# Performance work log

Hardware: AMD Instinct MI355X
Metric: run time of the kernel (lower is better)

## Reference

```python
import jax, jax.numpy as jnp
import numpy as np

NQ = 4            # num_qubits
DIM = 2 ** NQ     # 16-dim complex state

def _rx(theta):
    c = jnp.cos(theta / 2.0); s = jnp.sin(theta / 2.0)
    return jnp.array([[c, -1j * s], [-1j * s, c]], dtype=jnp.complex64)

def _ry(theta):
    c = jnp.cos(theta / 2.0); s = jnp.sin(theta / 2.0)
    return jnp.array([[c, -s], [s, c]], dtype=jnp.complex64)

def _apply_1q(state, q, U):
    # state: [B, 16] complex; apply 2x2 unitary U on qubit q (qubit 0 = MSB)
    B = state.shape[0]
    st = state.reshape((B,) + (2,) * NQ)
    st = jnp.moveaxis(st, 1 + q, -1)
    st = st @ U.T
    st = jnp.moveaxis(st, -1, 1 + q)
    return st.reshape(B, DIM)

def _apply_cnot(state, c, t):
    # flip target qubit t where control qubit c == 1
    B = state.shape[0]
    st = state.reshape((B,) + (2,) * NQ)
    st = jnp.moveaxis(st, (1 + c, 1 + t), (-2, -1))
    st = jnp.stack([st[..., 0, :], st[..., 1, ::-1]], axis=-2)
    st = jnp.moveaxis(st, (-2, -1), (1 + c, 1 + t))
    return st.reshape(B, DIM)

def _circuit(state):
    rx1, ry1 = _rx(0.1), _ry(0.2)
    rx2, ry2 = _rx(0.3), _ry(0.4)
    for q in range(NQ):
        state = _apply_1q(state, q, rx1)
        state = _apply_1q(state, q, ry1)
    for q in range(NQ - 1):
        state = _apply_cnot(state, q, q + 1)
    for q in range(NQ):
        state = _apply_1q(state, q, rx2)
        state = _apply_1q(state, q, ry2)
    return state

def setup_inputs() -> dict:
    key = jax.random.key(0)
    ks = jax.random.split(key, 9)
    B = 65536
    return {
        'x':   jax.random.normal(ks[0], (B, 784), dtype=jnp.float32),
        'We1': jax.random.normal(ks[1], (784, 256), dtype=jnp.float32) * 0.05,
        'be1': jnp.zeros((256,), dtype=jnp.float32),
        'We2': jax.random.normal(ks[2], (256, 32), dtype=jnp.float32) * 0.05,
        'be2': jnp.zeros((32,), dtype=jnp.float32),
        'W1':  jax.random.normal(ks[3], (32, 128), dtype=jnp.float32) * 0.05,
        'b1':  jnp.zeros((128,), dtype=jnp.float32),
        'W2':  jax.random.normal(ks[4], (128, 10), dtype=jnp.float32) * 0.05,
        'b2':  jnp.zeros((10,), dtype=jnp.float32),
    }

def reference(x, We1, be1, We2, be2, W1, b1, W2, b2):
    # encoder: Linear(784,256) -> ReLU -> Linear(256,32) -> Tanh
    h = jax.nn.relu(x @ We1 + be1)
    enc = jnp.tanh(h @ We2 + be2)               # [B, 32]
    psi = (enc[:, :DIM] + 1j * enc[:, DIM:]).astype(jnp.complex64)
    norm = jnp.sqrt(jnp.sum(jnp.abs(psi) ** 2, axis=1, keepdims=True))
    psi = psi / norm
    psi = _circuit(psi)                          # [B, 16] complex
    feat = jnp.concatenate([psi.real, psi.imag], axis=1)  # [B, 32]
    # classifier: Linear(32,128) -> ReLU -> (Dropout=identity in eval) -> Linear(128,10)
    out = jax.nn.relu(feat @ W1 + b1) @ W2 + b2
    return out
```

## Files before the change

kernel.cpp:

```cpp
#include <hip/hip_runtime.h>
#include <stdint.h>

#define DEVINL __device__ __forceinline__

typedef short bf16x8 __attribute__((ext_vector_type(8)));
typedef float f32x4  __attribute__((ext_vector_type(4)));

DEVINL uint16_t f2bf(float f) {
    uint32_t u = __builtin_bit_cast(uint32_t, f);
    uint32_t r = u + 0x7fffu + ((u >> 16) & 1u);
    return (uint16_t)(r >> 16);
}

DEVINL f32x4 mfma16x16x32(bf16x8 a, bf16x8 b, f32x4 c) {
    return __builtin_amdgcn_mfma_f32_16x16x32_bf16(a, b, c, 0, 0, 0);
}

#define WS_WE1T 0
#define WS_H    401408
#define WS_WE2T 33955840
#define WS_W1T  33972224
#define WS_W2T  33980416

__global__ __launch_bounds__(256) void prep_weights(
    const float* __restrict__ We1, const float* __restrict__ We2,
    const float* __restrict__ W1,  const float* __restrict__ W2,
    uint16_t* __restrict__ We1T, uint16_t* __restrict__ We2T,
    uint16_t* __restrict__ W1T,  uint16_t* __restrict__ W2T) {
    int tid = blockIdx.x * 256 + threadIdx.x;
    if (tid < 256 * 784) {
        int n = tid / 784, k = tid % 784;
        We1T[tid] = f2bf(We1[k * 256 + n]);
        return;
    }
    int t2 = tid - 256 * 784;
    if (t2 < 32 * 256) {
        int n = t2 / 256, k = t2 % 256;
        We2T[t2] = f2bf(We2[k * 32 + n]);
        return;
    }
    int t3 = t2 - 32 * 256;
    if (t3 < 128 * 32) {
        int n = t3 / 32, k = t3 % 32;
        W1T[t3] = f2bf(W1[k * 128 + n]);
        return;
    }
    int t4 = t3 - 128 * 32;
    if (t4 < 16 * 128) {
        int n = t4 / 128, k = t4 % 128;
        W2T[t4] = (n < 10) ? f2bf(W2[k * 10 + n]) : (uint16_t)0;
        return;
    }
}

__global__ __launch_bounds__(512) void gemm1_kernel(
    const float* __restrict__ x, const uint16_t* __restrict__ We1T,
    const float* __restrict__ be1, uint16_t* __restrict__ h) {
    __shared__ __align__(16) uint16_t Als[128 * 40];
    __shared__ __align__(16) uint16_t Bls[256 * 40];

    const int t = threadIdx.x;
    const int mbase = blockIdx.x * 128;
    const int w  = t >> 6;
    const int l  = t & 63;
    const int wm = w >> 2;
    const int wn = w & 3;
    const int lm = l & 15;
    const int lq = l >> 4;

    f32x4 acc[4][4] = {};

    const int ar = t >> 2;
    const int aq = t & 3;
    const int br = t >> 1;
    const int bh = t & 1;

    for (int k0 = 0; k0 < 784; k0 += 32) {
        {
            float4 v0 = {0.f,0.f,0.f,0.f}, v1 = {0.f,0.f,0.f,0.f};
            int c = k0 + aq * 8;
            if (c < 784) {
                const float* p = x + (size_t)(mbase + ar) * 784 + c;
                v0 = *(const float4*)p;
                v1 = *(const float4*)(p + 4);
            }
            union { uint4 u4; uint16_t us[8]; } pk;
            pk.us[0] = f2bf(v0.x); pk.us[1] = f2bf(v0.y);
            pk.us[2] = f2bf(v0.z); pk.us[3] = f2bf(v0.w);
            pk.us[4] = f2bf(v1.x); pk.us[5] = f2bf(v1.y);
            pk.us[6] = f2bf(v1.z); pk.us[7] = f2bf(v1.w);
            *(uint4*)&Als[ar * 40 + aq * 8] = pk.u4;
        }
        {
            int c = k0 + bh * 16;
            uint4 u0 = {0,0,0,0}, u1 = {0,0,0,0};
            if (c < 784) {
                const uint16_t* p = We1T + (size_t)br * 784 + c;
                u0 = *(const uint4*)p;
                u1 = *(const uint4*)(p + 8);
            }
            *(uint4*)&Bls[br * 40 + bh * 16]     = u0;
            *(uint4*)&Bls[br * 40 + bh * 16 + 8] = u1;
        }
        __syncthreads();

        bf16x8 afr[4], bfr[4];
        #pragma unroll
        for (int mi = 0; mi < 4; mi++)
            afr[mi] = *(const bf16x8*)&Als[(wm * 64 + mi * 16 + lm) * 40 + lq * 8];
        #pragma unroll
        for (int ni = 0; ni < 4; ni++)
            bfr[ni] = *(const bf16x8*)&Bls[(wn * 64 + ni * 16 + lm) * 40 + lq * 8];
        #pragma unroll
        for (int mi = 0; mi < 4; mi++)
            #pragma unroll
            for (int ni = 0; ni < 4; ni++)
                acc[mi][ni] = mfma16x16x32(afr[mi], bfr[ni], acc[mi][ni]);
        __syncthreads();
    }

    #pragma unroll
    for (int ni = 0; ni < 4; ni++) {
        int n = wn * 64 + ni * 16 + lm;
        float bias = be1[n];
        #pragma unroll
        for (int mi = 0; mi < 4; mi++) {
            #pragma unroll
            for (int i = 0; i < 4; i++) {
                int m = mbase + wm * 64 + mi * 16 + lq * 4 + i;
                float v = acc[mi][ni][i] + bias;
                v = v > 0.f ? v : 0.f;
                h[(size_t)m * 256 + n] = f2bf(v);
            }
        }
    }
}

DEVINL void apply_rx(float* sr, float* si, int bit, float c, float s) {
    #pragma unroll
    for (int i = 0; i < 16; i++) {
        if (!(i & bit)) {
            int j = i | bit;
            float r0 = sr[i], i0 = si[i], r1 = sr[j], i1 = si[j];
            sr[i] = c * r0 + s * i1;  si[i] = c * i0 - s * r1;
            sr[j] = c * r1 + s * i0;  si[j] = c * i1 - s * r0;
        }
    }
}
DEVINL void apply_ry(float* sr, float* si, int bit, float c, float s) {
    #pragma unroll
    for (int i = 0; i < 16; i++) {
        if (!(i & bit)) {
            int j = i | bit;
            float r0 = sr[i], i0 = si[i], r1 = sr[j], i1 = si[j];
            sr[i] = c * r0 - s * r1;  si[i] = c * i0 - s * i1;
            sr[j] = s * r0 + c * r1;  si[j] = s * i0 + c * i1;
        }
    }
}
DEVINL void apply_cnot(float* sr, float* si, int cb, int tb) {
    #pragma unroll
    for (int i = 0; i < 16; i++) {
        if ((i & cb) && !(i & tb)) {
            int j = i | tb;
            float tr = sr[i]; sr[i] = sr[j]; sr[j] = tr;
            float ti = si[i]; si[i] = si[j]; si[j] = ti;
        }
    }
}
DEVINL void circuit(float* sr, float* si) {
    const float C1 = 0.99875026039496628f, S1 = 0.04997916927067833f;
    const float C2 = 0.99500416527802582f, S2 = 0.09983341664682815f;
    const float C3 = 0.98877107793604227f, S3 = 0.14943813247359922f;
    const float C4 = 0.98006657784124163f, S4 = 0.19866933079506122f;
    #pragma unroll
    for (int q = 0; q < 4; q++) {
        int bit = 8 >> q;
        apply_rx(sr, si, bit, C1, S1);
        apply_ry(sr, si, bit, C2, S2);
    }
    apply_cnot(sr, si, 8, 4);
    apply_cnot(sr, si, 4, 2);
    apply_cnot(sr, si, 2, 1);
    #pragma unroll
    for (int q = 0; q < 4; q++) {
        int bit = 8 >> q;
        apply_rx(sr, si, bit, C3, S3);
        apply_ry(sr, si, bit, C4, S4);
    }
}

__global__ __launch_bounds__(256) void tail_kernel(
    const uint16_t* __restrict__ h, const uint16_t* __restrict__ We2T,
    const float* __restrict__ be2,
    const uint16_t* __restrict__ W1T, const float* __restrict__ b1,
    const uint16_t* __restrict__ W2T, const float* __restrict__ b2,
    float* __restrict__ out) {
    __shared__ __align__(16) uint16_t hls[64 * 264];
    __shared__ __align__(16) uint16_t we2ls[32 * 264];
    __shared__ __align__(16) uint16_t w1ls[128 * 40];
    __shared__ __align__(16) uint16_t w2ls[16 * 136];

    const int t = threadIdx.x;
    const int rowbase = blockIdx.x * 64;
    const int w  = t >> 6;
    const int l  = t & 63;
    const int lm = l & 15;
    const int lq = l >> 4;

    #pragma unroll
    for (int v = 0; v < 8; v++) {
        int c = t * 8 + v;
        int r = c >> 5, c8 = (c & 31) * 8;
        *(uint4*)&hls[r * 264 + c8] = *(const uint4*)&h[(size_t)(rowbase + r) * 256 + c8];
    }
    #pragma unroll
    for (int v = 0; v < 4; v++) {
        int c = t * 4 + v;
        int r = c >> 5, c8 = (c & 31) * 8;
        *(uint4*)&we2ls[r * 264 + c8] = *(const uint4*)&We2T[r * 256 + c8];
    }
    #pragma unroll
    for (int v = 0; v < 2; v++) {
        int c = t * 2 + v;
        int r = c >> 2, c8 = (c & 3) * 8;
        *(uint4*)&w1ls[r * 40 + c8] = *(const uint4*)&W1T[r * 32 + c8];
    }
    {
        int r = t >> 4, c8 = (t & 15) * 8;
        *(uint4*)&w2ls[r * 136 + c8] = *(const uint4*)&W2T[r * 128 + c8];
    }
    __syncthreads();

    f32x4 acc2[2] = {};
    #pragma unroll
    for (int k0 = 0; k0 < 256; k0 += 32) {
        bf16x8 af = *(const bf16x8*)&hls[(w * 16 + lm) * 264 + k0 + lq * 8];
        #pragma unroll
        for (int ni = 0; ni < 2; ni++) {
            bf16x8 bf = *(const bf16x8*)&we2ls[(ni * 16 + lm) * 264 + k0 + lq * 8];
            acc2[ni] = mfma16x16x32(af, bf, acc2[ni]);
        }
    }
    __syncthreads();

    float* encls = (float*)hls;
    uint16_t* featls = ((uint16_t*)hls) + 4224;
    uint16_t* a1ls   = ((uint16_t*)hls) + 6784;

    #pragma unroll
    for (int ni = 0; ni < 2; ni++) {
        int col = ni * 16 + lm;
        float bias = be2[col];
        #pragma unroll
        for (int i = 0; i < 4; i++) {
            int r = w * 16 + lq * 4 + i;
            encls[r * 33 + col] = tanhf(acc2[ni][i] + bias);
        }
    }
    __syncthreads();

    if (t < 64) {
        float e[32];
        #pragma unroll
        for (int j = 0; j < 32; j++) e[j] = encls[t * 33 + j];
        float s = 0.f;
        #pragma unroll
        for (int j = 0; j < 32; j++) s += e[j] * e[j];
        float inv = 1.0f / sqrtf(s);
        float sr[16], si[16];
        #pragma unroll
        for (int i = 0; i < 16; i++) { sr[i] = e[i] * inv; si[i] = e[16 + i] * inv; }
        circuit(sr, si);
        #pragma unroll
        for (int i = 0; i < 16; i++) {
            featls[t * 40 + i]      = f2bf(sr[i]);
            featls[t * 40 + 16 + i] = f2bf(si[i]);
        }
    }
    __syncthreads();

    f32x4 acc3[8] = {};
    {
        bf16x8 af = *(const bf16x8*)&featls[(w * 16 + lm) * 40 + lq * 8];
        #pragma unroll
        for (int ni = 0; ni < 8; ni++) {
            bf16x8 bf = *(const bf16x8*)&w1ls[(ni * 16 + lm) * 40 + lq * 8];
            acc3[ni] = mfma16x16x32(af, bf, acc3[ni]);
        }
    }
    #pragma unroll
    for (int ni = 0; ni < 8; ni++) {
        int col = ni * 16 + lm;
        float bias = b1[col];
        #pragma unroll
        for (int i = 0; i < 4; i++) {
            int r = w * 16 + lq * 4 + i;
            float v = acc3[ni][i] + bias;
            v = v > 0.f ? v : 0.f;
            a1ls[r * 136 + col] = f2bf(v);
        }
    }
    __syncthreads();

    f32x4 acc4 = {};
    #pragma unroll
    for (int k0 = 0; k0 < 128; k0 += 32) {
        bf16x8 af = *(const bf16x8*)&a1ls[(w * 16 + lm) * 136 + k0 + lq * 8];
        bf16x8 bf = *(const bf16x8*)&w2ls[lm * 136 + k0 + lq * 8];
        acc4 = mfma16x16x32(af, bf, acc4);
    }
    if (lm < 10) {
        float bias = b2[lm];
        #pragma unroll
        for (int i = 0; i < 4; i++) {
            int r = rowbase + w * 16 + lq * 4 + i;
            out[(size_t)r * 10 + lm] = acc4[i] + bias;
        }
    }
}

extern "C" void kernel_launch(void* const* d_in, const int* in_sizes, int n_in,
                              void* d_out, int out_size, void* d_ws, size_t ws_size,
                              hipStream_t stream) {
    const float* x   = (const float*)d_in[0];
    const float* We1 = (const float*)d_in[1];
    const float* be1 = (const float*)d_in[2];
    const float* We2 = (const float*)d_in[3];
    const float* be2 = (const float*)d_in[4];
    const float* W1  = (const float*)d_in[5];
    const float* b1  = (const float*)d_in[6];
    const float* W2  = (const float*)d_in[7];
    const float* b2  = (const float*)d_in[8];
    float* out = (float*)d_out;

    char* ws = (char*)d_ws;
    uint16_t* We1T = (uint16_t*)(ws + WS_WE1T);
    uint16_t* hbuf = (uint16_t*)(ws + WS_H);
    uint16_t* We2T = (uint16_t*)(ws + WS_WE2T);
    uint16_t* W1T  = (uint16_t*)(ws + WS_W1T);
    uint16_t* W2T  = (uint16_t*)(ws + WS_W2T);

    hipLaunchKernelGGL(prep_weights, dim3(840), dim3(256), 0, stream,
                       We1, We2, W1, W2, We1T, We2T, W1T, W2T);
    hipLaunchKernelGGL(gemm1_kernel, dim3(512), dim3(512), 0, stream,
                       x, We1T, be1, hbuf);
    hipLaunchKernelGGL(tail_kernel, dim3(1024), dim3(256), 0, stream,
                       hbuf, We2T, be2, W1T, b1, W2T, b2, out);
}
```

Before: 338.4 us.

## Use async global-to-LDS loads for weights and register-prefetch x in gemm1

Pads the transposed bf16 encoder weight to K=800 so every tile is full. The weight tile now goes straight from global memory into LDS with global_load_lds, instead of passing through registers. The next x tile is prefetched into registers while the current tile is converted and stored, and one barrier per iteration is dropped. The LDS row padding (stride 40) is removed to suit the async load layout, which may add bank conflicts on fragment reads, and a launch-bounds occupancy hint is added.

```diff
diff --git a/kernel.cpp b/kernel.cpp
--- a/kernel.cpp
+++ b/kernel.cpp
@@ -16,11 +16,17 @@
     return __builtin_amdgcn_mfma_f32_16x16x32_bf16(a, b, c, 0, 0, 0);
 }
 
+DEVINL void async_load16(const void* g, void* l) {
+    __builtin_amdgcn_global_load_lds(
+        (const __attribute__((address_space(1))) void*)g,
+        (__attribute__((address_space(3))) void*)l, 16, 0, 0);
+}
+
 #define WS_WE1T 0
-#define WS_H    401408
-#define WS_WE2T 33955840
-#define WS_W1T  33972224
-#define WS_W2T  33980416
+#define WS_H    409600
+#define WS_WE2T 33964032
+#define WS_W1T  33980416
+#define WS_W2T  33988608
 
 __global__ __launch_bounds__(256) void prep_weights(
     const float* __restrict__ We1, const float* __restrict__ We2,
@@ -28,12 +34,12 @@
     uint16_t* __restrict__ We1T, uint16_t* __restrict__ We2T,
     uint16_t* __restrict__ W1T,  uint16_t* __restrict__ W2T) {
     int tid = blockIdx.x * 256 + threadIdx.x;
-    if (tid < 256 * 784) {
-        int n = tid / 784, k = tid % 784;
-        We1T[tid] = f2bf(We1[k * 256 + n]);
+    if (tid < 256 * 800) {
+        int n = tid / 800, k = tid % 800;
+        We1T[tid] = (k < 784) ? f2bf(We1[k * 256 + n]) : (uint16_t)0;
         return;
     }
-    int t2 = tid - 256 * 784;
+    int t2 = tid - 256 * 800;
     if (t2 < 32 * 256) {
         int n = t2 / 256, k = t2 % 256;
         We2T[t2] = f2bf(We2[k * 32 + n]);
@@ -53,11 +59,11 @@
     }
 }
 
-__global__ __launch_bounds__(512) void gemm1_kernel(
+__global__ __launch_bounds__(512, 4) void gemm1_kernel(
     const float* __restrict__ x, const uint16_t* __restrict__ We1T,
     const float* __restrict__ be1, uint16_t* __restrict__ h) {
-    __shared__ __align__(16) uint16_t Als[128 * 40];
-    __shared__ __align__(16) uint16_t Bls[256 * 40];
+    __shared__ __align__(16) uint16_t Als[128 * 32];
+    __shared__ __align__(16) uint16_t Bls[256 * 32];
 
     const int t = threadIdx.x;
     const int mbase = blockIdx.x * 128;
@@ -72,51 +78,56 @@
 
     const int ar = t >> 2;
     const int aq = t & 3;
-    const int br = t >> 1;
-    const int bh = t & 1;
-
-    for (int k0 = 0; k0 < 784; k0 += 32) {
+    const float* xrow = x + (size_t)(mbase + ar) * 784;
+
+    const int g1 = t, g2 = 512 + t;
+    const uint16_t* bp1 = We1T + (size_t)(g1 >> 2) * 800 + (g1 & 3) * 8;
+    const uint16_t* bp2 = We1T + (size_t)(g2 >> 2) * 800 + (g2 & 3) * 8;
+
+    float4 va0 = *(const float4*)(xrow + aq * 8);
+    float4 va1 = *(const float4*)(xrow + aq * 8 + 4);
+
+    for (int k0 = 0; k0 < 800; k0 += 32) {
+        __syncthreads();
+
+        async_load16(bp1 + k0, &Bls[8 * g1]);
+        async_load16(bp2 + k0, &Bls[8 * g2]);
+
+        union { uint4 u4; uint16_t us[8]; } pk;
+        pk.us[0] = f2bf(va0.x); pk.us[1] = f2bf(va0.y);
+        pk.us[2] = f2bf(va0.z); pk.us[3] = f2bf(va0.w);
+        pk.us[4] = f2bf(va1.x); pk.us[5] = f2bf(va1.y);
+        pk.us[6] = f2bf(va1.z); pk.us[7] = f2bf(va1.w);
+        *(uint4*)&Als[8 * t] = pk.u4;
+
         {
-            float4 v0 = {0.f,0.f,0.f,0.f}, v1 = {0.f,0.f,0.f,0.f};
-            int c = k0 + aq * 8;
-            if (c < 784) {
-                const float* p = x + (size_t)(mbase + ar) * 784 + c;
-                v0 = *(const float4*)p;
-                v1 = *(const float4*)(p + 4);
+            int kn = k0 + 32;
+            if (kn < 800) {
+                int c = kn + aq * 8;
+                if (c < 784) {
+                    va0 = *(const float4*)(xrow + c);
+                    va1 = *(const float4*)(xrow + c + 4);
+                } else {
+                    va0 = make_float4(0.f, 0.f, 0.f, 0.f);
+                    va1 = make_float4(0.f, 0.f, 0.f, 0.f);
+                }
             }
-            union { uint4 u4; uint16_t us[8]; } pk;
-            pk.us[0] = f2bf(v0.x); pk.us[1] = f2bf(v0.y);
-            pk.us[2] = f2bf(v0.z); pk.us[3] = f2bf(v0.w);
-            pk.us[4] = f2bf(v1.x); pk.us[5] = f2bf(v1.y);
-            pk.us[6] = f2bf(v1.z); pk.us[7] = f2bf(v1.w);
-            *(uint4*)&Als[ar * 40 + aq * 8] = pk.u4;
-        }
-        {
-            int c = k0 + bh * 16;
-            uint4 u0 = {0,0,0,0}, u1 = {0,0,0,0};
-            if (c < 784) {
-                const uint16_t* p = We1T + (size_t)br * 784 + c;
-                u0 = *(const uint4*)p;
-                u1 = *(const uint4*)(p + 8);
-            }
-            *(uint4*)&Bls[br * 40 + bh * 16]     = u0;
-            *(uint4*)&Bls[br * 40 + bh * 16 + 8] = u1;
-        }
+        }
+
         __syncthreads();
 
         bf16x8 afr[4], bfr[4];
         #pragma unroll
         for (int mi = 0; mi < 4; mi++)
-            afr[mi] = *(const bf16x8*)&Als[(wm * 64 + mi * 16 + lm) * 40 + lq * 8];
+            afr[mi] = *(const bf16x8*)&Als[(wm * 64 + mi * 16 + lm) * 32 + lq * 8];
         #pragma unroll
         for (int ni = 0; ni < 4; ni++)
-            bfr[ni] = *(const bf16x8*)&Bls[(wn * 64 + ni * 16 + lm) * 40 + lq * 8];
+            bfr[ni] = *(const bf16x8*)&Bls[(wn * 64 + ni * 16 + lm) * 32 + lq * 8];
         #pragma unroll
         for (int mi = 0; mi < 4; mi++)
             #pragma unroll
             for (int ni = 0; ni < 4; ni++)
                 acc[mi][ni] = mfma16x16x32(afr[mi], bfr[ni], acc[mi][ni]);
-        __syncthreads();
     }
 
     #pragma unroll
@@ -341,7 +352,7 @@
     uint16_t* W1T  = (uint16_t*)(ws + WS_W1T);
     uint16_t* W2T  = (uint16_t*)(ws + WS_W2T);
 
-    hipLaunchKernelGGL(prep_weights, dim3(840), dim3(256), 0, stream,
+    hipLaunchKernelGGL(prep_weights, dim3(856), dim3(256), 0, stream,
                        We1, We2, W1, W2, We1T, We2T, W1T, W2T);
     hipLaunchKernelGGL(gemm1_kernel, dim3(512), dim3(512), 0, stream,
                        x, We1T, be1, hbuf);
```

Measured after the change: 333.2 us. Within noise of the previous version (-1.6%).
